# Kernel optimization log

Measured on AMD Instinct MI355X. Metric: run time of the kernel, lower is better.

The kernel has to match this reference:

```python
import jax, jax.numpy as jnp
from jax import lax
import numpy as np

# init_kwargs (FlowNet-C canonical config)
K = 1      # kernel_size
MD = 20    # max_displacement
S1 = 1     # stride_1 (input stride)
S2 = 2     # stride_2 (displacement stride)
PAD = 20   # spatial zero padding


def setup_inputs() -> dict:
    key = jax.random.key(0)
    k1, k2 = jax.random.split(key)
    shape = (16, 48, 64, 256)  # [B, H, W, C], channels_last
    return {
        "input_a": jax.random.normal(k1, shape, dtype=jnp.float32),
        "input_b": jax.random.normal(k2, shape, dtype=jnp.float32),
    }


def _corr(a, b):
    # FlowNet correlation cost volume (TFA addons_correlation_cost semantics).
    B, H, W, C = a.shape
    rad = MD // S2                      # displacement radius in stride_2 steps
    D = 2 * rad + 1                     # displacements per axis
    rk = (K - 1) // 2                   # kernel radius
    bd = MD + rk                        # border
    oH = H + 2 * (PAD - bd) // S1       # matches layer's compute_output_shape
    oW = W + 2 * (PAD - bd) // S1
    rows = (oH - 1) * S1 + K            # extent of input needed (pre-pool)
    cols = (oW - 1) * S1 + K

    pa = jnp.pad(a, ((0, 0), (PAD, PAD), (PAD, PAD), (0, 0)))
    pb = jnp.pad(b, ((0, 0), (PAD, PAD), (PAD, PAD), (0, 0)))
    # static region of A covering all kernel windows (centers at h*S1+bd)
    a_reg = lax.slice(pa, (0, bd - rk, bd - rk, 0),
                      (B, bd - rk + rows, bd - rk + cols, C))

    def body(_, d):
        # top_channel d -> (tj, ti) row-major, tj vertical as in TFA kernel
        dy = (d // D) * S2 - MD
        dx = (d % D) * S2 - MD
        b_reg = lax.dynamic_slice(pb, (0, bd - rk + dy, bd - rk + dx, 0),
                                  (B, rows, cols, C))
        p = jnp.sum(a_reg * b_reg, axis=-1)           # [B, rows, cols]
        o = lax.reduce_window(p, 0.0, lax.add,
                              (1, K, K), (1, S1, S1), 'VALID')  # [B, oH, oW]
        return None, o

    # remat keeps scan residuals small (slices recomputed in any backward pass)
    _, outs = lax.scan(jax.checkpoint(body), None, jnp.arange(D * D))
    # [D*D, B, oH, oW] -> [B, oH, oW, D*D]; TFA kernel divides by K*K*C
    return jnp.transpose(outs, (1, 2, 3, 0)) / (K * K * C)


def reference(input_a, input_b):
    return _corr(input_a, input_b)
```

## Files before the change

### kernel.cpp

```cpp
#include <hip/hip_runtime.h>
#include <hip/hip_bf16.h>

#define HH    48
#define WW    64
#define CC    256
#define ND    21
#define OUTD  441
#define PITCH 264
#define SROWS 32

typedef __bf16 v8bf16 __attribute__((ext_vector_type(8)));
typedef float  v4f    __attribute__((ext_vector_type(4)));

__global__ __launch_bounds__(384)
void corr_mfma_kernel(const float* __restrict__ A, const float* __restrict__ B,
                      float* __restrict__ out) {
    __shared__ __bf16 Blds[2][SROWS * PITCH];

    const int blk  = blockIdx.x;
    const int b    = blk >> 6;
    const int rem  = blk & 63;
    const int ck   = rem & 1;
    const int p    = (rem >> 1) & 1;
    const int hpar = (rem >> 2) & 1;
    const int trip = rem >> 3;
    const int h0   = 6 * trip + hpar;

    const int tid  = threadIdx.x;
    const int lane = tid & 63;
    const int wave = tid >> 6;
    const int mt   = wave & 1;
    const int hr   = wave >> 1;
    const int n    = lane & 15;
    const int quad = lane >> 4;

    const int h = h0 + 2 * hr;

    const int i_lo_f = (h0 >= 21) ? 0 : ((21 - h0) >> 1);
    const int i_hi_f = min(22, (67 - h0) >> 1);
    const int i_mid  = (i_lo_f + i_hi_f + 1) >> 1;
    const int i_lo   = ck ? i_mid : i_lo_f;
    const int i_hi   = ck ? i_hi_f : (i_mid - 1);

    for (int r = 0; r < 3; ++r) {
        int hrow = h0 + 2 * r;
        int z_lo, z_hi;
        if (ck == 0) { z_lo = 0;                      z_hi = min(20, i_lo_f - r - 1); }
        else         { z_lo = max(0, i_hi_f - r + 1); z_hi = 20; }
        float* outr = out + (size_t)(b * HH + hrow) * WW * OUTD;
        for (int tj = z_lo; tj <= z_hi; ++tj) {
            for (int idx = tid; idx < 32 * ND; idx += 384) {
                int wp = idx / ND, ti = idx - wp * ND;
                int w  = (wp << 1) + p;
                outr[(size_t)w * OUTD + tj * ND + ti] = 0.f;
            }
        }
    }

    v8bf16 afrag[8];
    {
        int w_a = ((mt * 16 + n) << 1) + p;
        const float* arow = A + ((size_t)(b * HH + h) * WW + w_a) * CC;
        #pragma unroll
        for (int kc = 0; kc < 8; ++kc) {
            int c0 = kc * 32 + quad * 8;
            float4 f0 = *(const float4*)(arow + c0);
            float4 f1 = *(const float4*)(arow + c0 + 4);
            v8bf16 af;
            af[0] = (__bf16)f0.x; af[1] = (__bf16)f0.y; af[2] = (__bf16)f0.z; af[3] = (__bf16)f0.w;
            af[4] = (__bf16)f1.x; af[5] = (__bf16)f1.y; af[6] = (__bf16)f1.z; af[7] = (__bf16)f1.w;
            afrag[kc] = af;
        }
    }

    const float* bimg = B + (size_t)(b * HH) * WW * CC + p * CC;
    float4 pf[6];
    auto load_pf = [&](int hb) {
        const float* brow = bimg + (size_t)hb * WW * CC;
        #pragma unroll
        for (int it = 0; it < 6; ++it) {
            int idx = it * 384 + tid;
            if (idx < 2048)
                pf[it] = *(const float4*)(brow + (idx >> 6) * 2 * CC + ((idx & 63) << 2));
        }
    };
    auto store_lds = [&](int buf) {
        #pragma unroll
        for (int it = 0; it < 6; ++it) {
            int idx = it * 384 + tid;
            if (idx < 2048) {
                __bf16* dst = &Blds[buf][(idx >> 6) * PITCH + ((idx & 63) << 2)];
                dst[0] = (__bf16)pf[it].x; dst[1] = (__bf16)pf[it].y;
                dst[2] = (__bf16)pf[it].z; dst[3] = (__bf16)pf[it].w;
            }
        }
    };

    load_pf(h0 - 20 + 2 * i_lo);
    store_lds(0);
    int cur = 0;

    float* outr = out + (size_t)(b * HH + h) * WW * OUTD;

    for (int i = i_lo; i <= i_hi; ++i) {
        if (i < i_hi) load_pf(h0 - 20 + 2 * (i + 1));
        __syncthreads();

        const int tj = i - hr;
        if ((unsigned)tj <= 20u) {
            const __bf16* bbase = &Blds[cur][n * PITCH + quad * 8];
            v4f acc0 = {0.f, 0.f, 0.f, 0.f};
            v4f acc1 = acc0;
            #pragma unroll
            for (int kc = 0; kc < 8; ++kc) {
                v8bf16 bf0 = *(const v8bf16*)(bbase + kc * 32);
                v8bf16 bf1 = *(const v8bf16*)(bbase + 16 * PITCH + kc * 32);
                acc0 = __builtin_amdgcn_mfma_f32_16x16x32_bf16(afrag[kc], bf0, acc0, 0, 0, 0);
                acc1 = __builtin_amdgcn_mfma_f32_16x16x32_bf16(afrag[kc], bf1, acc1, 0, 0, 0);
            }
            #pragma unroll
            for (int r = 0; r < 4; ++r) {
                int wp = mt * 16 + quad * 4 + r;
                int w  = (wp << 1) + p;
                float* orow = outr + (size_t)w * OUTD + tj * ND;
                int ti0 = 10 + n - wp;
                if ((unsigned)ti0 < 21u) orow[ti0] = acc0[r] * (1.f / 256.f);
                int ti1 = 26 + n - wp;
                if ((unsigned)ti1 < 21u) orow[ti1] = acc1[r] * (1.f / 256.f);
                if (n < 10 - wp)  orow[n]      = 0.f;
                if (n <= wp - 22) orow[20 - n] = 0.f;
            }
        }

        if (i < i_hi) store_lds(cur ^ 1);
        cur ^= 1;
    }
}

extern "C" void kernel_launch(void* const* d_in, const int* in_sizes, int n_in,
                              void* d_out, int out_size, void* d_ws, size_t ws_size,
                              hipStream_t stream) {
    const float* A = (const float*)d_in[0];
    const float* B = (const float*)d_in[1];
    float* out = (float*)d_out;
    dim3 grid(16 * 64);
    dim3 block(384);
    corr_mfma_kernel<<<grid, block, 0, stream>>>(A, B, out);
}
```

Before: 212.2 us.

## Process six output rows per block to reuse each staged B row twice

Result: faster. 206.7 us (-2.6%).

```diff
diff --git a/kernel.cpp b/kernel.cpp
--- a/kernel.cpp
+++ b/kernel.cpp
@@ -10,6 +10,7 @@
 #define SROWS 32
 
 typedef __bf16 v8bf16 __attribute__((ext_vector_type(8)));
+typedef __bf16 v4bf16 __attribute__((ext_vector_type(4)));
 typedef float  v4f    __attribute__((ext_vector_type(4)));
 
 __global__ __launch_bounds__(384)
@@ -18,60 +19,27 @@
     __shared__ __bf16 Blds[2][SROWS * PITCH];
 
     const int blk  = blockIdx.x;
-    const int b    = blk >> 6;
-    const int rem  = blk & 63;
+    const int b    = blk >> 5;
+    const int rem  = blk & 31;
     const int ck   = rem & 1;
     const int p    = (rem >> 1) & 1;
     const int hpar = (rem >> 2) & 1;
-    const int trip = rem >> 3;
-    const int h0   = 6 * trip + hpar;
+    const int grp  = rem >> 3;
+    const int h0   = hpar + 12 * grp;
 
     const int tid  = threadIdx.x;
     const int lane = tid & 63;
     const int wave = tid >> 6;
     const int mt   = wave & 1;
-    const int hr   = wave >> 1;
+    const int hg   = wave >> 1;
     const int n    = lane & 15;
     const int quad = lane >> 4;
 
-    const int h = h0 + 2 * hr;
-
-    const int i_lo_f = (h0 >= 21) ? 0 : ((21 - h0) >> 1);
-    const int i_hi_f = min(22, (67 - h0) >> 1);
+    const int i_lo_f = (h0 >= 20) ? 0 : ((21 - h0) >> 1);
+    const int i_hi_f = min(25, (67 - h0) >> 1);
     const int i_mid  = (i_lo_f + i_hi_f + 1) >> 1;
     const int i_lo   = ck ? i_mid : i_lo_f;
     const int i_hi   = ck ? i_hi_f : (i_mid - 1);
-
-    for (int r = 0; r < 3; ++r) {
-        int hrow = h0 + 2 * r;
-        int z_lo, z_hi;
-        if (ck == 0) { z_lo = 0;                      z_hi = min(20, i_lo_f - r - 1); }
-        else         { z_lo = max(0, i_hi_f - r + 1); z_hi = 20; }
-        float* outr = out + (size_t)(b * HH + hrow) * WW * OUTD;
-        for (int tj = z_lo; tj <= z_hi; ++tj) {
-            for (int idx = tid; idx < 32 * ND; idx += 384) {
-                int wp = idx / ND, ti = idx - wp * ND;
-                int w  = (wp << 1) + p;
-                outr[(size_t)w * OUTD + tj * ND + ti] = 0.f;
-            }
-        }
-    }
-
-    v8bf16 afrag[8];
-    {
-        int w_a = ((mt * 16 + n) << 1) + p;
-        const float* arow = A + ((size_t)(b * HH + h) * WW + w_a) * CC;
-        #pragma unroll
-        for (int kc = 0; kc < 8; ++kc) {
-            int c0 = kc * 32 + quad * 8;
-            float4 f0 = *(const float4*)(arow + c0);
-            float4 f1 = *(const float4*)(arow + c0 + 4);
-            v8bf16 af;
-            af[0] = (__bf16)f0.x; af[1] = (__bf16)f0.y; af[2] = (__bf16)f0.z; af[3] = (__bf16)f0.w;
-            af[4] = (__bf16)f1.x; af[5] = (__bf16)f1.y; af[6] = (__bf16)f1.z; af[7] = (__bf16)f1.w;
-            afrag[kc] = af;
-        }
-    }
 
     const float* bimg = B + (size_t)(b * HH) * WW * CC + p * CC;
     float4 pf[6];
@@ -89,47 +57,91 @@
         for (int it = 0; it < 6; ++it) {
             int idx = it * 384 + tid;
             if (idx < 2048) {
-                __bf16* dst = &Blds[buf][(idx >> 6) * PITCH + ((idx & 63) << 2)];
-                dst[0] = (__bf16)pf[it].x; dst[1] = (__bf16)pf[it].y;
-                dst[2] = (__bf16)pf[it].z; dst[3] = (__bf16)pf[it].w;
+                v4bf16 t;
+                t[0] = (__bf16)pf[it].x; t[1] = (__bf16)pf[it].y;
+                t[2] = (__bf16)pf[it].z; t[3] = (__bf16)pf[it].w;
+                *(v4bf16*)&Blds[buf][(idx >> 6) * PITCH + ((idx & 63) << 2)] = t;
             }
         }
     };
 
     load_pf(h0 - 20 + 2 * i_lo);
+
+    for (int r = 0; r < 6; ++r) {
+        int z_lo, z_hi;
+        if (ck == 0) { z_lo = 0;                      z_hi = min(20, i_lo_f - r - 1); }
+        else         { z_lo = max(0, i_hi_f - r + 1); z_hi = 20; }
+        if (z_lo > z_hi) continue;
+        float* outr = out + (size_t)(b * HH + h0 + 2 * r) * WW * OUTD;
+        for (int tj = z_lo; tj <= z_hi; ++tj) {
+            for (int idx = tid; idx < 32 * ND; idx += 384) {
+                int wp = idx / ND, ti = idx - wp * ND;
+                int w  = (wp << 1) + p;
+                outr[(size_t)w * OUTD + tj * ND + ti] = 0.f;
+            }
+        }
+    }
+
+    v8bf16 afrag[2][8];
+    {
+        int w_a = ((mt * 16 + n) << 1) + p;
+        #pragma unroll
+        for (int rr = 0; rr < 2; ++rr) {
+            int h = h0 + 4 * hg + 2 * rr;
+            const float* arow = A + ((size_t)(b * HH + h) * WW + w_a) * CC;
+            #pragma unroll
+            for (int kc = 0; kc < 8; ++kc) {
+                int c0 = kc * 32 + quad * 8;
+                float4 f0 = *(const float4*)(arow + c0);
+                float4 f1 = *(const float4*)(arow + c0 + 4);
+                v8bf16 af;
+                af[0] = (__bf16)f0.x; af[1] = (__bf16)f0.y; af[2] = (__bf16)f0.z; af[3] = (__bf16)f0.w;
+                af[4] = (__bf16)f1.x; af[5] = (__bf16)f1.y; af[6] = (__bf16)f1.z; af[7] = (__bf16)f1.w;
+                afrag[rr][kc] = af;
+            }
+        }
+    }
+
     store_lds(0);
     int cur = 0;
 
-    float* outr = out + (size_t)(b * HH + h) * WW * OUTD;
+    auto epilogue = [&](const v4f& acc0, const v4f& acc1, int h, int tj) {
+        float* outr = out + (size_t)(b * HH + h) * WW * OUTD;
+        #pragma unroll
+        for (int q = 0; q < 4; ++q) {
+            int wp = mt * 16 + quad * 4 + q;
+            int w  = (wp << 1) + p;
+            float* orow = outr + (size_t)w * OUTD + tj * ND;
+            int ti0 = 10 + n - wp;
+            if ((unsigned)ti0 < 21u) orow[ti0] = acc0[q] * (1.f / 256.f);
+            int ti1 = 26 + n - wp;
+            if ((unsigned)ti1 < 21u) orow[ti1] = acc1[q] * (1.f / 256.f);
+            if (n < 10 - wp)  orow[n]      = 0.f;
+            if (n <= wp - 22) orow[20 - n] = 0.f;
+        }
+    };
 
     for (int i = i_lo; i <= i_hi; ++i) {
         if (i < i_hi) load_pf(h0 - 20 + 2 * (i + 1));
         __syncthreads();
 
-        const int tj = i - hr;
-        if ((unsigned)tj <= 20u) {
+        const int tj0 = i - 2 * hg;
+        if ((unsigned)tj0 <= 21u) {
             const __bf16* bbase = &Blds[cur][n * PITCH + quad * 8];
-            v4f acc0 = {0.f, 0.f, 0.f, 0.f};
-            v4f acc1 = acc0;
+            v4f a00 = {0.f, 0.f, 0.f, 0.f};
+            v4f a01 = a00, a10 = a00, a11 = a00;
             #pragma unroll
             for (int kc = 0; kc < 8; ++kc) {
                 v8bf16 bf0 = *(const v8bf16*)(bbase + kc * 32);
                 v8bf16 bf1 = *(const v8bf16*)(bbase + 16 * PITCH + kc * 32);
-                acc0 = __builtin_amdgcn_mfma_f32_16x16x32_bf16(afrag[kc], bf0, acc0, 0, 0, 0);
-                acc1 = __builtin_amdgcn_mfma_f32_16x16x32_bf16(afrag[kc], bf1, acc1, 0, 0, 0);
+                a00 = __builtin_amdgcn_mfma_f32_16x16x32_bf16(afrag[0][kc], bf0, a00, 0, 0, 0);
+                a01 = __builtin_amdgcn_mfma_f32_16x16x32_bf16(afrag[0][kc], bf1, a01, 0, 0, 0);
+                a10 = __builtin_amdgcn_mfma_f32_16x16x32_bf16(afrag[1][kc], bf0, a10, 0, 0, 0);
+                a11 = __builtin_amdgcn_mfma_f32_16x16x32_bf16(afrag[1][kc], bf1, a11, 0, 0, 0);
             }
-            #pragma unroll
-            for (int r = 0; r < 4; ++r) {
-                int wp = mt * 16 + quad * 4 + r;
-                int w  = (wp << 1) + p;
-                float* orow = outr + (size_t)w * OUTD + tj * ND;
-                int ti0 = 10 + n - wp;
-                if ((unsigned)ti0 < 21u) orow[ti0] = acc0[r] * (1.f / 256.f);
-                int ti1 = 26 + n - wp;
-                if ((unsigned)ti1 < 21u) orow[ti1] = acc1[r] * (1.f / 256.f);
-                if (n < 10 - wp)  orow[n]      = 0.f;
-                if (n <= wp - 22) orow[20 - n] = 0.f;
-            }
+            if ((unsigned)tj0 <= 20u)       epilogue(a00, a01, h0 + 4 * hg,     tj0);
+            const int tj1 = tj0 - 1;
+            if ((unsigned)tj1 <= 20u)       epilogue(a10, a11, h0 + 4 * hg + 2, tj1);
         }
 
         if (i < i_hi) store_lds(cur ^ 1);
@@ -143,7 +155,7 @@
     const float* A = (const float*)d_in[0];
     const float* B = (const float*)d_in[1];
     float* out = (float*)d_out;
-    dim3 grid(16 * 64);
+    dim3 grid(16 * 32);
     dim3 block(384);
     corr_mfma_kernel<<<grid, block, 0, stream>>>(A, B, out);
 }
```
